# Performance work log

Hardware: AMD Instinct MI355X
Metric: run time of the kernel (lower is better)

Reference implementation:

```python
import jax, jax.numpy as jnp
import numpy as np

B, C, H, W = 8, 256, 64, 64
HEADS, H_SP, W_SP = 8, 64, 4  # idx=0: H_sp=resolution[0], W_sp=split_size
D = C // HEADS
SCALE = D ** -0.5
HH, WW = H // H_SP, W // W_SP  # 1, 16 (no padding needed)


def setup_inputs() -> dict:
    key = jax.random.key(0)
    k1, k2, k3 = jax.random.split(key, 3)
    temp = jax.random.normal(k1, (B, 3, C, H, W), dtype=jnp.float32)
    get_v_weight = jax.random.normal(k2, (C, 1, 3, 3), dtype=jnp.float32) * 0.1
    get_v_bias = jax.random.normal(k3, (C,), dtype=jnp.float32) * 0.1
    return {"temp": temp, "get_v_weight": get_v_weight, "get_v_bias": get_v_bias}


def _im2win_shuffle(x):
    # x: (B, C, H, W); H split as (H_SP, HH) with H_SP OUTER (shuffled windows)
    x = x.reshape(B, HEADS, D, H_SP, HH, W_SP, WW)
    x = x.transpose(0, 4, 6, 1, 3, 5, 2)  # b hh ww h H_sp W_sp d
    return x.reshape(B * HH * WW, HEADS, H_SP * W_SP, D)


def reference(temp, get_v_weight, get_v_bias):
    # H, W are multiples of H_SP, W_SP -> pad is zero (faithful to F.pad path)
    q, k, v = temp[:, 0], temp[:, 1], temp[:, 2]
    qw = _im2win_shuffle(q) * SCALE
    kw = _im2win_shuffle(k)
    vw = _im2win_shuffle(v)

    # LePE: depthwise 3x3 conv applied per shuffled window
    vimg = v.reshape(B, C, H_SP, HH, W_SP, WW).transpose(0, 3, 5, 1, 2, 4)
    vimg = vimg.reshape(B * HH * WW, C, H_SP, W_SP)
    lepe = jax.lax.conv_general_dilated(
        vimg, get_v_weight, (1, 1), ((1, 1), (1, 1)),
        dimension_numbers=("NCHW", "OIHW", "NCHW"), feature_group_count=C,
    ) + get_v_bias[None, :, None, None]
    lepe = lepe.reshape(B * HH * WW, HEADS, D, H_SP * W_SP).transpose(0, 1, 3, 2)

    attn = jax.nn.softmax(jnp.einsum("whqd,whkd->whqk", qw, kw), axis=-1)
    x = jnp.einsum("whqk,whkd->whqd", attn, vw) + lepe  # (nW, h, S, d)

    # windows2img_shuffle -> (B, C, H, W), then raw .view to (B, H, W, C)
    x = x.reshape(B, HH, WW, HEADS, H_SP, W_SP, D)
    x = x.transpose(0, 3, 6, 4, 1, 5, 2).reshape(B, C, H, W)
    x = x.reshape(B, H, W, C)  # raw memory view, matches torch .view
    return x.reshape(B, H * W, C)
```

## Files before the change

kernel.cpp:

```cpp
#include <hip/hip_runtime.h>


typedef __attribute__((ext_vector_type(8))) short bf16x8;
typedef __attribute__((ext_vector_type(4))) float floatx4;
typedef unsigned short ushort_t;
typedef unsigned int uint_t;

constexpr float QSCALE = 0.25503486f;

__device__ __forceinline__ ushort_t f2bf(float f) {
    union { float f; uint_t u; } v; v.f = f;
    uint_t r = v.u + 0x7fffu + ((v.u >> 16) & 1u);
    return (ushort_t)(r >> 16);
}
__device__ __forceinline__ float bf2f(ushort_t h) {
    union { uint_t u; float f; } v; v.u = ((uint_t)h) << 16;
    return v.f;
}
__device__ __forceinline__ float bfu2f(uint_t bits) {
    union { uint_t u; float f; } v; v.u = bits; return v.f;
}
__device__ __forceinline__ uint_t cvtpk(float lo, float hi) {
    uint_t r;
    asm("v_cvt_pk_bf16_f32 %0, %1, %2" : "=v"(r) : "v"(lo), "v"(hi));
    return r;
}

constexpr int KP    = 1280;
constexpr int VBASE = 16 * KP;
constexpr int VP    = 1280;
constexpr int SMU   = VBASE + 16 * VP;
constexpr int LSTR  = 2432;
constexpr int OSTR  = 1058;

template<bool SCALE>
__device__ __forceinline__ void stage_kq(const float4* __restrict__ src,
                                         ushort_t* dst, int u, int hb) {
    const int w4 = u & 15, h8 = (u >> 4) & 7, d = (u >> 7) * 4;
    union F4 { float4 v; float a[4]; } v0, v1, v2, v3;
    const size_t base = (size_t)(hb + h8) * 16 + w4;
    v0.v = src[(size_t)(d + 0) * 1024 + base];
    v1.v = src[(size_t)(d + 1) * 1024 + base];
    v2.v = src[(size_t)(d + 2) * 1024 + base];
    v3.v = src[(size_t)(d + 3) * 1024 + base];
    const int tl = h8 * 4 + (w4 >> 2), a = w4 & 3;
    #pragma unroll
    for (int j = 0; j < 4; j++) {
        uint_t lo, hi;
        if (SCALE) {
            lo = cvtpk(v0.a[j] * QSCALE, v1.a[j] * QSCALE);
            hi = cvtpk(v2.a[j] * QSCALE, v3.a[j] * QSCALE);
        } else {
            lo = cvtpk(v0.a[j], v1.a[j]);
            hi = cvtpk(v2.a[j], v3.a[j]);
        }
        uint2 pk; pk.x = lo; pk.y = hi;
        *(uint2*)&dst[(a * 4 + j) * KP + tl * 40 + d] = pk;
    }
}

__global__ __launch_bounds__(1024) __attribute__((amdgpu_waves_per_eu(8)))
void fused_kernel(const float* __restrict__ temp, const float* __restrict__ wgt,
                  const float* __restrict__ bias, float* __restrict__ out)
{
    const int bid = blockIdx.x;
    const int hd = bid & 7;
    const int qq = (bid >> 3) & 3;
    const int b  = bid >> 5;

    __shared__ __align__(16) ushort_t SM[SMU];

    const int u = threadIdx.x;
    const int w8 = u >> 6;
    const int ln = u & 63;
    const int lm = ln & 15, q4 = ln >> 4;

    const float4* Tq4 = (const float4*)temp + ((size_t)((b * 3 + 0) * 256 + hd * 32)) * 1024;
    const float4* Tk4 = Tq4 + (size_t)256 * 1024;
    const float4* Tv4 = Tk4 + (size_t)256 * 1024;

    bf16x8 qa[4];
    #pragma unroll
    for (int pass = 0; pass < 2; pass++) {
        stage_kq<true>(Tq4, SM, u, qq * 16 + pass * 8);
        __syncthreads();
        #pragma unroll
        for (int Tl = 0; Tl < 2; Tl++)
            qa[pass * 2 + Tl] = *(const bf16x8*)&SM[w8 * KP + (Tl * 16 + lm) * 40 + q4 * 8];
        __syncthreads();
    }

    floatx4 acc[4][2];
    float lsum[4];
    #pragma unroll
    for (int T = 0; T < 4; T++) {
        acc[T][0] = (floatx4)0.0f; acc[T][1] = (floatx4)0.0f;
        lsum[T] = 0.0f;
    }

    const int k0row = ((lm >> 2) << 3) + (lm & 3);
    const int pKb = w8 * KP;
    const int pVb = VBASE + w8 * VP;

    for (int kt = 0; kt < 8; kt++) {
        stage_kq<false>(Tk4, SM, u, kt * 8);
        {
            const int a = u & 3, h8 = (u >> 2) & 7, dv = u >> 5;
            union F4 { float4 v; float a[4]; } w0, w1, w2, w3;
            const size_t vb = (size_t)dv * 1024 + (size_t)(kt * 8 + h8) * 16 + a;
            w0.v = Tv4[vb];  w1.v = Tv4[vb + 4];  w2.v = Tv4[vb + 8];  w3.v = Tv4[vb + 12];
            #pragma unroll
            for (int j = 0; j < 4; j++) {
                uint2 pk;
                pk.x = cvtpk(w0.a[j], w1.a[j]);
                pk.y = cvtpk(w2.a[j], w3.a[j]);
                *(uint2*)&SM[VBASE + (a * 4 + j) * VP + dv * 40 + h8 * 4] = pk;
            }
        }
        __syncthreads();

        const bf16x8 kb0 = *(const bf16x8*)&SM[pKb + k0row * 40 + q4 * 8];
        const bf16x8 kb1 = *(const bf16x8*)&SM[pKb + (k0row + 4) * 40 + q4 * 8];
        const bf16x8 vb0 = *(const bf16x8*)&SM[pVb + lm * 40 + q4 * 8];
        const bf16x8 vb1 = *(const bf16x8*)&SM[pVb + (16 + lm) * 40 + q4 * 8];
        #pragma unroll
        for (int T = 0; T < 4; T++) {
            floatx4 s0 = __builtin_amdgcn_mfma_f32_16x16x32_bf16(kb0, qa[T], (floatx4)0.0f, 0, 0, 0);
            floatx4 s1 = __builtin_amdgcn_mfma_f32_16x16x32_bf16(kb1, qa[T], (floatx4)0.0f, 0, 0, 0);
            const uint_t u0 = cvtpk(exp2f(s0[0]), exp2f(s0[1]));
            const uint_t u1 = cvtpk(exp2f(s0[2]), exp2f(s0[3]));
            const uint_t u2 = cvtpk(exp2f(s1[0]), exp2f(s1[1]));
            const uint_t u3 = cvtpk(exp2f(s1[2]), exp2f(s1[3]));
            lsum[T] += bfu2f(u0 << 16) + bfu2f(u0 & 0xffff0000u)
                     + bfu2f(u1 << 16) + bfu2f(u1 & 0xffff0000u)
                     + bfu2f(u2 << 16) + bfu2f(u2 & 0xffff0000u)
                     + bfu2f(u3 << 16) + bfu2f(u3 & 0xffff0000u);
            union { uint_t w[4]; bf16x8 v; } pa;
            pa.w[0] = u0; pa.w[1] = u1; pa.w[2] = u2; pa.w[3] = u3;
            acc[T][0] = __builtin_amdgcn_mfma_f32_16x16x32_bf16(pa.v, vb0, acc[T][0], 0, 0, 0);
            acc[T][1] = __builtin_amdgcn_mfma_f32_16x16x32_bf16(pa.v, vb1, acc[T][1], 0, 0, 0);
        }
        __syncthreads();
    }

    #pragma unroll
    for (int i = 0; i < 9; i++) {
        const int flat = i * 1024 + u;
        const int f4w = flat & 15, rowid = flat >> 4;
        const int d = rowid / 18, hl = rowid - d * 18;
        const int hh = qq * 16 - 1 + hl;
        union F4 { float4 v; float a[4]; } v;
        if ((unsigned)hh < 64u) v.v = Tv4[(size_t)d * 1024 + hh * 16 + f4w];
        else { v.a[0] = 0.f; v.a[1] = 0.f; v.a[2] = 0.f; v.a[3] = 0.f; }
        const int cx = f4w >> 2, wb = (f4w & 3) * 4;
        #pragma unroll
        for (int j = 0; j < 4; j++)
            SM[(wb + j) * LSTR + d * 76 + hl * 4 + cx] = f2bf(v.a[j]);
    }
    __syncthreads();

    float wc[2][9], bs2[2];
    #pragma unroll
    for (int dt = 0; dt < 2; dt++) {
        const int d = dt * 16 + lm;
        #pragma unroll
        for (int k = 0; k < 9; k++) wc[dt][k] = wgt[(hd * 32 + d) * 9 + k];
        bs2[dt] = bias[hd * 32 + d];
    }

    #pragma unroll
    for (int T = 0; T < 4; T++) {
        float tot = lsum[T];
        tot += __shfl_xor(tot, 16);
        tot += __shfl_xor(tot, 32);
        float inv[4];
        #pragma unroll
        for (int r = 0; r < 4; r++) inv[r] = 1.0f / __shfl(tot, q4 * 4 + r);

        #pragma unroll
        for (int dt = 0; dt < 2; dt++) {
            const int d = dt * 16 + lm;
            float vv[3][4];
            #pragma unroll
            for (int dy = 0; dy < 3; dy++) {
                const int hl = T * 4 + q4 + dy;
                #pragma unroll
                for (int cx = 0; cx < 4; cx++)
                    vv[dy][cx] = bf2f(SM[w8 * LSTR + d * 76 + hl * 4 + cx]);
            }
            #pragma unroll
            for (int r = 0; r < 4; r++) {
                float lep = bs2[dt];
                #pragma unroll
                for (int dy = 0; dy < 3; dy++) {
                    #pragma unroll
                    for (int kx = 0; kx < 3; kx++) {
                        const int wsrc = r + kx - 1;
                        if (wsrc >= 0 && wsrc < 4) lep += wc[dt][dy * 3 + kx] * vv[dy][wsrc];
                    }
                }
                acc[T][dt][r] = acc[T][dt][r] * inv[r] + lep;
            }
        }
    }
    __syncthreads();

    float* Ob = (float*)SM;
    float4* out4 = (float4*)out + ((size_t)(b * 256 + hd * 32)) * 1024;
    #pragma unroll
    for (int half = 0; half < 2; half++) {
        #pragma unroll
        for (int Tl = 0; Tl < 2; Tl++) {
            const int T = half * 2 + Tl;
            #pragma unroll
            for (int dt = 0; dt < 2; dt++) {
                #pragma unroll
                for (int r = 0; r < 4; r++)
                    Ob[w8 * OSTR + (Tl * 16 + q4 * 4 + r) * 33 + dt * 16 + lm] = acc[T][dt][r];
            }
        }
        __syncthreads();
        #pragma unroll
        for (int i = 0; i < 4; i++) {
            const int flat = i * 1024 + u;
            const int f4 = flat & 3, ql = (flat >> 2) & 31, dd = flat >> 7;
            float4 o;
            o.x = Ob[(f4 * 4 + 0) * OSTR + ql * 33 + dd];
            o.y = Ob[(f4 * 4 + 1) * OSTR + ql * 33 + dd];
            o.z = Ob[(f4 * 4 + 2) * OSTR + ql * 33 + dd];
            o.w = Ob[(f4 * 4 + 3) * OSTR + ql * 33 + dd];
            out4[(size_t)dd * 1024 + (qq * 64 + half * 32 + ql) * 4 + f4] = o;
        }
        __syncthreads();
    }
}

extern "C" void kernel_launch(void* const* d_in, const int* in_sizes, int n_in,
                              void* d_out, int out_size, void* d_ws, size_t ws_size,
                              hipStream_t stream) {
    const float* temp = (const float*)d_in[0];
    const float* wgt  = (const float*)d_in[1];
    const float* bias = (const float*)d_in[2];
    float* out = (float*)d_out;
    (void)d_ws; (void)ws_size;
    fused_kernel<<<dim3(256), dim3(1024), 0, stream>>>(temp, wgt, bias, out);
}
```

Before: 239.0 us.

## Split work across 1024 blocks of 256 threads instead of 256 blocks of 1024

The grid is now indexed over window-column groups (wq), so each block handles 4 windows instead of 16, with 256 threads and a quarter of the shared memory. Each block gets smaller staging loops for Q, K, V and the LePE tile, and the output transpose is done per T tile. The intent is to fill all CUs (256 blocks underuse a 256-CU part) and raise occupancy through smaller blocks and less LDS. The cost is that each block issues narrower, strided global loads (single float4 per row per window column), which may reduce coalescing, and it runs more barriers per unit of work.

Measured after the change: 245.9 us. 2.9% more time.

```diff
diff --git a/kernel.cpp b/kernel.cpp
--- a/kernel.cpp
+++ b/kernel.cpp
@@ -27,66 +27,53 @@
 }
 
 constexpr int KP    = 1280;
-constexpr int VBASE = 16 * KP;
+constexpr int VBASE = 4 * KP;
 constexpr int VP    = 1280;
-constexpr int SMU   = VBASE + 16 * VP;
-constexpr int LSTR  = 2432;
-constexpr int OSTR  = 1058;
-
-template<bool SCALE>
-__device__ __forceinline__ void stage_kq(const float4* __restrict__ src,
-                                         ushort_t* dst, int u, int hb) {
-    const int w4 = u & 15, h8 = (u >> 4) & 7, d = (u >> 7) * 4;
-    union F4 { float4 v; float a[4]; } v0, v1, v2, v3;
-    const size_t base = (size_t)(hb + h8) * 16 + w4;
-    v0.v = src[(size_t)(d + 0) * 1024 + base];
-    v1.v = src[(size_t)(d + 1) * 1024 + base];
-    v2.v = src[(size_t)(d + 2) * 1024 + base];
-    v3.v = src[(size_t)(d + 3) * 1024 + base];
-    const int tl = h8 * 4 + (w4 >> 2), a = w4 & 3;
-    #pragma unroll
-    for (int j = 0; j < 4; j++) {
-        uint_t lo, hi;
-        if (SCALE) {
-            lo = cvtpk(v0.a[j] * QSCALE, v1.a[j] * QSCALE);
-            hi = cvtpk(v2.a[j] * QSCALE, v3.a[j] * QSCALE);
-        } else {
-            lo = cvtpk(v0.a[j], v1.a[j]);
-            hi = cvtpk(v2.a[j], v3.a[j]);
-        }
-        uint2 pk; pk.x = lo; pk.y = hi;
-        *(uint2*)&dst[(a * 4 + j) * KP + tl * 40 + d] = pk;
-    }
-}
-
-__global__ __launch_bounds__(1024) __attribute__((amdgpu_waves_per_eu(8)))
+constexpr int SMU   = VBASE + 4 * VP;
+constexpr int LDP   = 74;
+constexpr int LPS   = 32 * LDP;
+constexpr int OPS   = 530;
+
+__global__ __launch_bounds__(256, 6)
 void fused_kernel(const float* __restrict__ temp, const float* __restrict__ wgt,
                   const float* __restrict__ bias, float* __restrict__ out)
 {
     const int bid = blockIdx.x;
     const int hd = bid & 7;
-    const int qq = (bid >> 3) & 3;
-    const int b  = bid >> 5;
+    const int b  = (bid >> 3) & 7;
+    const int wq = (bid >> 6) & 3;
+    const int qq = bid >> 8;
 
     __shared__ __align__(16) ushort_t SM[SMU];
 
     const int u = threadIdx.x;
-    const int w8 = u >> 6;
+    const int w = u >> 6;
     const int ln = u & 63;
     const int lm = ln & 15, q4 = ln >> 4;
 
-    const float4* Tq4 = (const float4*)temp + ((size_t)((b * 3 + 0) * 256 + hd * 32)) * 1024;
+    const float4* Tq4 = (const float4*)temp + ((size_t)((b * 3 + 0) * 256 + hd * 32)) * 1024 + wq;
     const float4* Tk4 = Tq4 + (size_t)256 * 1024;
     const float4* Tv4 = Tk4 + (size_t)256 * 1024;
 
+    union F4 { float4 v; float a[4]; };
+
     bf16x8 qa[4];
     #pragma unroll
-    for (int pass = 0; pass < 2; pass++) {
-        stage_kq<true>(Tq4, SM, u, qq * 16 + pass * 8);
-        __syncthreads();
-        #pragma unroll
-        for (int Tl = 0; Tl < 2; Tl++)
-            qa[pass * 2 + Tl] = *(const bf16x8*)&SM[w8 * KP + (Tl * 16 + lm) * 40 + q4 * 8];
+    for (int pass = 0; pass < 4; pass++) {
+        {
+            const int tq = u & 15, d2 = u >> 4;
+            const int d = d2 * 2;
+            const int tg = qq * 64 + pass * 16 + tq;
+            F4 v0, v1;
+            v0.v = Tq4[(size_t)d * 1024 + tg * 4];
+            v1.v = Tq4[(size_t)(d + 1) * 1024 + tg * 4];
+            #pragma unroll
+            for (int j = 0; j < 4; j++)
+                *(uint_t*)&SM[j * KP + tq * 40 + d] =
+                    cvtpk(v0.a[j] * QSCALE, v1.a[j] * QSCALE);
+        }
+        __syncthreads();
+        qa[pass] = *(const bf16x8*)&SM[w * KP + lm * 40 + q4 * 8];
         __syncthreads();
     }
 
@@ -99,23 +86,32 @@
     }
 
     const int k0row = ((lm >> 2) << 3) + (lm & 3);
-    const int pKb = w8 * KP;
-    const int pVb = VBASE + w8 * VP;
+    const int pKb = w * KP;
+    const int pVb = VBASE + w * VP;
 
     for (int kt = 0; kt < 8; kt++) {
-        stage_kq<false>(Tk4, SM, u, kt * 8);
-        {
-            const int a = u & 3, h8 = (u >> 2) & 7, dv = u >> 5;
-            union F4 { float4 v; float a[4]; } w0, w1, w2, w3;
-            const size_t vb = (size_t)dv * 1024 + (size_t)(kt * 8 + h8) * 16 + a;
-            w0.v = Tv4[vb];  w1.v = Tv4[vb + 4];  w2.v = Tv4[vb + 8];  w3.v = Tv4[vb + 12];
-            #pragma unroll
-            for (int j = 0; j < 4; j++) {
-                uint2 pk;
-                pk.x = cvtpk(w0.a[j], w1.a[j]);
-                pk.y = cvtpk(w2.a[j], w3.a[j]);
-                *(uint2*)&SM[VBASE + (a * 4 + j) * VP + dv * 40 + h8 * 4] = pk;
-            }
+        #pragma unroll
+        for (int i = 0; i < 2; i++) {
+            const int flat = i * 256 + u;
+            const int k = flat & 31, d2 = flat >> 5;
+            const int d = d2 * 2;
+            F4 v0, v1;
+            v0.v = Tk4[(size_t)d * 1024 + (kt * 32 + k) * 4];
+            v1.v = Tk4[(size_t)(d + 1) * 1024 + (kt * 32 + k) * 4];
+            #pragma unroll
+            for (int j = 0; j < 4; j++)
+                *(uint_t*)&SM[j * KP + k * 40 + d] = cvtpk(v0.a[j], v1.a[j]);
+        }
+        #pragma unroll
+        for (int i = 0; i < 2; i++) {
+            const int flat = i * 256 + u;
+            const int k2 = flat & 15, dv = flat >> 4;
+            F4 va, vb;
+            va.v = Tv4[(size_t)dv * 1024 + (kt * 32 + k2 * 2) * 4];
+            vb.v = Tv4[(size_t)dv * 1024 + (kt * 32 + k2 * 2 + 1) * 4];
+            #pragma unroll
+            for (int j = 0; j < 4; j++)
+                *(uint_t*)&SM[VBASE + j * VP + dv * 40 + k2 * 2] = cvtpk(va.a[j], vb.a[j]);
         }
         __syncthreads();
 
@@ -135,8 +131,8 @@
                      + bfu2f(u1 << 16) + bfu2f(u1 & 0xffff0000u)
                      + bfu2f(u2 << 16) + bfu2f(u2 & 0xffff0000u)
                      + bfu2f(u3 << 16) + bfu2f(u3 & 0xffff0000u);
-            union { uint_t w[4]; bf16x8 v; } pa;
-            pa.w[0] = u0; pa.w[1] = u1; pa.w[2] = u2; pa.w[3] = u3;
+            union { uint_t pw[4]; bf16x8 v; } pa;
+            pa.pw[0] = u0; pa.pw[1] = u1; pa.pw[2] = u2; pa.pw[3] = u3;
             acc[T][0] = __builtin_amdgcn_mfma_f32_16x16x32_bf16(pa.v, vb0, acc[T][0], 0, 0, 0);
             acc[T][1] = __builtin_amdgcn_mfma_f32_16x16x32_bf16(pa.v, vb1, acc[T][1], 0, 0, 0);
         }
@@ -145,17 +141,17 @@
 
     #pragma unroll
     for (int i = 0; i < 9; i++) {
-        const int flat = i * 1024 + u;
-        const int f4w = flat & 15, rowid = flat >> 4;
-        const int d = rowid / 18, hl = rowid - d * 18;
+        const int flat = i * 256 + u;
+        const int wsp = flat & 3;
+        const int rem = flat >> 2;
+        const int d = rem / 18, hl = rem - d * 18;
         const int hh = qq * 16 - 1 + hl;
-        union F4 { float4 v; float a[4]; } v;
-        if ((unsigned)hh < 64u) v.v = Tv4[(size_t)d * 1024 + hh * 16 + f4w];
+        F4 v;
+        if ((unsigned)hh < 64u) v.v = Tv4[(size_t)d * 1024 + hh * 16 + wsp * 4];
         else { v.a[0] = 0.f; v.a[1] = 0.f; v.a[2] = 0.f; v.a[3] = 0.f; }
-        const int cx = f4w >> 2, wb = (f4w & 3) * 4;
         #pragma unroll
         for (int j = 0; j < 4; j++)
-            SM[(wb + j) * LSTR + d * 76 + hl * 4 + cx] = f2bf(v.a[j]);
+            SM[j * LPS + d * LDP + hl * 4 + wsp] = f2bf(v.a[j]);
     }
     __syncthreads();
 
@@ -186,7 +182,7 @@
                 const int hl = T * 4 + q4 + dy;
                 #pragma unroll
                 for (int cx = 0; cx < 4; cx++)
-                    vv[dy][cx] = bf2f(SM[w8 * LSTR + d * 76 + hl * 4 + cx]);
+                    vv[dy][cx] = bf2f(SM[w * LPS + d * LDP + hl * 4 + cx]);
             }
             #pragma unroll
             for (int r = 0; r < 4; r++) {
@@ -206,30 +202,26 @@
     __syncthreads();
 
     float* Ob = (float*)SM;
-    float4* out4 = (float4*)out + ((size_t)(b * 256 + hd * 32)) * 1024;
-    #pragma unroll
-    for (int half = 0; half < 2; half++) {
-        #pragma unroll
-        for (int Tl = 0; Tl < 2; Tl++) {
-            const int T = half * 2 + Tl;
-            #pragma unroll
-            for (int dt = 0; dt < 2; dt++) {
-                #pragma unroll
-                for (int r = 0; r < 4; r++)
-                    Ob[w8 * OSTR + (Tl * 16 + q4 * 4 + r) * 33 + dt * 16 + lm] = acc[T][dt][r];
-            }
-        }
-        __syncthreads();
-        #pragma unroll
-        for (int i = 0; i < 4; i++) {
-            const int flat = i * 1024 + u;
-            const int f4 = flat & 3, ql = (flat >> 2) & 31, dd = flat >> 7;
+    float4* out4 = (float4*)out + ((size_t)(b * 256 + hd * 32)) * 1024 + wq;
+    #pragma unroll
+    for (int T = 0; T < 4; T++) {
+        #pragma unroll
+        for (int dt = 0; dt < 2; dt++) {
+            #pragma unroll
+            for (int r = 0; r < 4; r++)
+                Ob[w * OPS + (q4 * 4 + r) * 33 + dt * 16 + lm] = acc[T][dt][r];
+        }
+        __syncthreads();
+        #pragma unroll
+        for (int i = 0; i < 2; i++) {
+            const int flat = i * 256 + u;
+            const int q = flat & 15, d = flat >> 4;
             float4 o;
-            o.x = Ob[(f4 * 4 + 0) * OSTR + ql * 33 + dd];
-            o.y = Ob[(f4 * 4 + 1) * OSTR + ql * 33 + dd];
-            o.z = Ob[(f4 * 4 + 2) * OSTR + ql * 33 + dd];
-            o.w = Ob[(f4 * 4 + 3) * OSTR + ql * 33 + dd];
-            out4[(size_t)dd * 1024 + (qq * 64 + half * 32 + ql) * 4 + f4] = o;
+            o.x = Ob[0 * OPS + q * 33 + d];
+            o.y = Ob[1 * OPS + q * 33 + d];
+            o.z = Ob[2 * OPS + q * 33 + d];
+            o.w = Ob[3 * OPS + q * 33 + d];
+            out4[(size_t)d * 1024 + (qq * 64 + T * 16 + q) * 4] = o;
         }
         __syncthreads();
     }
@@ -243,5 +235,5 @@
     const float* bias = (const float*)d_in[2];
     float* out = (float*)d_out;
     (void)d_ws; (void)ws_size;
-    fused_kernel<<<dim3(256), dim3(1024), 0, stream>>>(temp, wgt, bias, out);
-}
+    fused_kernel<<<dim3(1024), dim3(256), 0, stream>>>(temp, wgt, bias, out);
+}
```
